# Optimization experiments

Hardware: AMD Instinct MI355X
Metric: run time of the kernel (lower is better)

Reference implementation:

```python
import jax, jax.numpy as jnp
import numpy as np

B, D, C, L, H, HF, HG, NCLS = 4096, 2048, 16, 128, 256, 512, 128, 200

def _init(key, shape, fan_in):
    return jax.random.normal(key, shape, dtype=jnp.float32) * (1.0 / np.sqrt(fan_in))

def setup_inputs() -> dict:
    key = jax.random.key(0)
    ks = jax.random.split(key, 16)
    return {
        "x": jax.random.normal(ks[0], (B, D), dtype=jnp.float32),
        "fp": jax.random.uniform(ks[1], (C, D), minval=-1.0, maxval=1.0, dtype=jnp.float32),  # probability_vector_logits
        "mean_inputs": jax.random.normal(ks[2], (D,), dtype=jnp.float32) * 0.1,
        "Wg1": _init(ks[3], (C, D, H), D), "bg1": jnp.zeros((C, H), jnp.float32),
        "Wg2": _init(ks[4], (C, H, L), H), "bg2": jnp.zeros((C, L), jnp.float32),
        "Wf1": _init(ks[5], (D, HF), D), "bf1": jnp.zeros((HF,), jnp.float32),
        "Wf2": _init(ks[6], (HF, L), HF), "bf2": jnp.zeros((L,), jnp.float32),
        "Wg_head": _init(ks[7], (C * (L // 2), HG), C * (L // 2)), "bg_head": jnp.zeros((HG,), jnp.float32),
        "Wc": _init(ks[8], (HG, NCLS), HG), "bc": jnp.zeros((NCLS,), jnp.float32),
    }

def _l2_normalize(v, axis):
    # tf.math.l2_normalize: v * rsqrt(max(sum(v^2), 1e-12))
    sq = jnp.sum(v * v, axis=axis, keepdims=True)
    return v * jax.lax.rsqrt(jnp.maximum(sq, 1e-12))

def reference(x, fp, mean_inputs, Wg1, bg1, Wg2, bg2, Wf1, bf1, Wf2, bf2, Wg_head, bg_head, Wc, bc):
    # Deterministic forward (training=False, forward_deterministic=True)
    gate = jax.nn.sigmoid(fp)  # [C, D]
    # mask_features: gate*x + (1-gate)*mean, vectorized over concepts -> [C, B, D]
    masked = gate[:, None, :] * x[None, :, :] + (1.0 - gate)[:, None, :] * mean_inputs[None, None, :]
    # per-concept generator MLPs (distinct weights per concept) -> concept_matrix [B, C, L]
    h = jax.nn.relu(jnp.einsum('cbd,cdh->cbh', masked, Wg1) + bg1[:, None, :])
    cm = jnp.einsum('cbh,chl->cbl', h, Wg2) + bg2[:, None, :]
    cm = jnp.transpose(cm, (1, 0, 2))              # [B, C, L]
    cm_norm = _l2_normalize(cm, axis=1)            # normalize across concept axis (axis=1 in TF code)
    # shared features_to_concepts model applied to each masked_x -> latent [C, B, L]
    hf = jax.nn.relu(jnp.einsum('cbd,dh->cbh', masked, Wf1) + bf1)
    latent = jnp.einsum('cbh,hl->cbl', hf, Wf2) + bf2
    latent = jnp.transpose(latent, (1, 0, 2))      # [B, C, L]
    # concept scores: sigmoid(<cm_norm[b,c,:], latent[b,c,:]>)
    concept_prob = jax.nn.sigmoid(jnp.sum(cm_norm * latent, axis=-1))  # [B, C]
    half = L // 2
    p = concept_prob[:, :, None]
    bottleneck = p * cm_norm[:, :, half:] + (1.0 - p) * cm_norm[:, :, :half]  # [B, C, L/2]
    bottleneck = bottleneck.reshape(bottleneck.shape[0], -1)                   # [B, C*L/2]
    # g_model + concepts_to_labels head
    z = jax.nn.relu(bottleneck @ Wg_head + bg_head)
    logits = z @ Wc + bc  # [B, NCLS]
    return logits
```

## Files before the change

kernel.cpp:

```cpp
#include <hip/hip_runtime.h>
#include <hip/hip_bf16.h>

typedef __bf16 bf16;
typedef __attribute__((ext_vector_type(8))) __bf16 bf16x8;
typedef __attribute__((ext_vector_type(4))) float f32x4;

__device__ __forceinline__ void gload_lds16(const void* g, void* l) {
    __builtin_amdgcn_global_load_lds(
        (const __attribute__((address_space(1))) unsigned int*)g,
        (__attribute__((address_space(3))) unsigned int*)l, 16, 0, 0);
}

#define BARRIER()   asm volatile("s_barrier" ::: "memory")
#define WAITLGKM0() asm volatile("s_waitcnt lgkmcnt(0)" ::: "memory")
#define WAITVM4()   asm volatile("s_waitcnt vmcnt(4)" ::: "memory")
#define WAITVM0()   asm volatile("s_waitcnt vmcnt(0)" ::: "memory")
#define SCHED0()    __builtin_amdgcn_sched_barrier(0)

__device__ __forceinline__ unsigned int pack2(float a, float b) {
    bf16 x = (bf16)a, y = (bf16)b;
    unsigned short ux, uy;
    __builtin_memcpy(&ux, &x, 2); __builtin_memcpy(&uy, &y, 2);
    return (unsigned int)ux | ((unsigned int)uy << 16);
}


__global__ void cvt_x(const float* __restrict__ in, bf16* __restrict__ out) {
    const long i = ((long)blockIdx.x * 256 + threadIdx.x) * 8;
    float4 v0 = *(const float4*)(in + i);
    float4 v1 = *(const float4*)(in + i + 4);
    bf16x8 o;
    o[0]=(bf16)v0.x; o[1]=(bf16)v0.y; o[2]=(bf16)v0.z; o[3]=(bf16)v0.w;
    o[4]=(bf16)v1.x; o[5]=(bf16)v1.y; o[6]=(bf16)v1.z; o[7]=(bf16)v1.w;
    *(bf16x8*)(out + i) = o;
}

__global__ void prep_gmv(const float* __restrict__ fp, const float* __restrict__ mean,
                         float* __restrict__ gmv) {
    const int i = blockIdx.x * 256 + threadIdx.x;
    const float g = 1.f / (1.f + expf(-fp[i]));
    gmv[i] = (1.f - g) * mean[i & 2047];
}

template <int SHARED_W>
__global__ void corr_kernel(const float* __restrict__ W, const float* __restrict__ gmv,
                            float* __restrict__ corr, int S) {
    __shared__ float red[4][64];
    const int c = blockIdx.y;
    const int sl = threadIdx.x & 63;
    const int s = blockIdx.x * 64 + sl;
    const int w = threadIdx.x >> 6;
    const float* Wc = W + (SHARED_W ? 0 : (long)c * 2048 * S);
    const float* gm = gmv + c * 2048;
    float acc = 0.f;
#pragma unroll 4
    for (int r = w; r < 2048; r += 4)
        acc = fmaf(gm[r], Wc[(long)r * S + s], acc);
    red[w][sl] = acc;
    __syncthreads();
    if (w == 0)
        corr[(long)c * S + s] = red[0][sl] + red[1][sl] + red[2][sl] + red[3][sl];
}

__global__ void prep_big(const float* __restrict__ Wg1, const float* __restrict__ Wf1,
                         bf16* __restrict__ Wall, const float* __restrict__ fp)
{
    __shared__ float tile[32][33];
    const int z = blockIdx.z;
    const int bx = blockIdx.x;
    const int r0 = blockIdx.y * 32;
    const int tx = threadIdx.x & 31, ty = threadIdx.x >> 5;
    const float* in; bf16* out; int S, s0;
    if (bx < 8) { S = 256; s0 = bx * 32; in = Wg1 + (long)z * 2048 * 256;
                  out = Wall + (long)z * 768 * 2048; }
    else        { S = 512; s0 = (bx - 8) * 32; in = Wf1;
                  out = Wall + (long)z * 768 * 2048 + (long)256 * 2048; }
#pragma unroll
    for (int i = 0; i < 32; i += 8)
        tile[ty + i][tx] = in[(long)(r0 + ty + i) * S + s0 + tx];
    __syncthreads();
    const float gv = 1.f / (1.f + expf(-fp[z * 2048 + r0 + tx]));
#pragma unroll
    for (int i = 0; i < 32; i += 8)
        out[(long)(s0 + ty + i) * 2048 + r0 + tx] = (bf16)(gv * tile[tx][ty + i]);
}

__global__ void prep_small(const float* __restrict__ Wg2, bf16* __restrict__ Wg2T,
                           const float* __restrict__ Wf2, bf16* __restrict__ Wf2T,
                           const float* __restrict__ Wgh, bf16* __restrict__ WghT)
{
    __shared__ float tile[32][33];
    const int b = blockIdx.x;
    const float* in; bf16* out; int R, bx, by;
    if (b < 512) {
        const int z = b >> 5, rem = b & 31;
        bx = rem & 3; by = rem >> 2; R = 256;
        in = Wg2 + (long)z * 256 * 128; out = Wg2T + (long)z * 128 * 256;
    } else if (b < 576) {
        const int rem = b - 512;
        bx = rem & 3; by = rem >> 2; R = 512;
        in = Wf2; out = Wf2T;
    } else {
        const int rem = b - 576;
        bx = rem & 3; by = rem >> 2; R = 1024;
        in = Wgh; out = WghT;
    }
    const int s0 = bx * 32, r0 = by * 32;
    const int tx = threadIdx.x & 31, ty = threadIdx.x >> 5;
#pragma unroll
    for (int i = 0; i < 32; i += 8)
        tile[ty + i][tx] = in[(long)(r0 + ty + i) * 128 + s0 + tx];
    __syncthreads();
#pragma unroll
    for (int i = 0; i < 32; i += 8)
        out[(long)(s0 + ty + i) * R + r0 + tx] = (bf16)tile[tx][ty + i];
}

__global__ __launch_bounds__(512, 2)
void gemm256(const bf16* __restrict__ A, const bf16* __restrict__ Wall,
             const float* __restrict__ bg1, const float* __restrict__ corr_g,
             const float* __restrict__ bf1, const float* __restrict__ corr_f,
             bf16* __restrict__ h_out, bf16* __restrict__ hf_out)
{
    __shared__ __align__(16) bf16 lds[2][4][8192];

    const int bid = blockIdx.x;
    const int swz = (bid & 7) * 96 + (bid >> 3);
    const int c   = swz / 48;
    const int rem = swz % 48;
    const int ny  = rem / 16;
    const int m0  = (rem % 16) * 256;

    const int t = threadIdx.x, lane = t & 63, w = t >> 6;
    const int wr = w >> 2, wc = w & 3;
    const bf16* Bc = Wall + (long)c * 768 * 2048;

    const int rr = lane >> 3;
    const int qq = (lane & 7) ^ rr;
    const bf16* pA0 = A  + (long)(m0 + w * 16 + rr) * 2048 + qq * 8;
    const bf16* pA1 = pA0 + 8 * 2048;
    const bf16* pB0 = Bc + (long)(ny * 256 + w * 16 + rr) * 2048 + qq * 8;
    const bf16* pB1 = pB0 + 8 * 2048;

    const int l15 = lane & 15;
    const int q0 = (((lane >> 4) ^ (lane & 7))) * 8;
    const int aoff0 = l15 * 64 + q0, aoff1 = aoff0 ^ 32;
    const int boff0 = ((wc & 1) * 64 + l15) * 64 + q0, boff1 = boff0 ^ 32;
    const int hb = 2 + (wc >> 1);

    f32x4 acc[8][4] = {};
    bf16x8 Ax[4][2], Ay[4][2], Bx[2][2], By[2][2];

#define STG(buf, half, P0, P1, e) do { \
    gload_lds16((P0) + (e), &lds[buf][half][w * 1024]); \
    gload_lds16((P1) + (e), &lds[buf][half][w * 1024 + 512]); } while (0)

#define RDA(dst, buf, mb) do { _Pragma("unroll") \
    for (int mm = 0; mm < 4; ++mm) { \
        dst[mm][0] = *(const bf16x8*)&lds[buf][wr][aoff0 + (mb + mm) * 1024]; \
        dst[mm][1] = *(const bf16x8*)&lds[buf][wr][aoff1 + (mb + mm) * 1024]; } } while (0)

#define RDB(dst, buf, nh) do { _Pragma("unroll") \
    for (int nn = 0; nn < 2; ++nn) { \
        dst[nn][0] = *(const bf16x8*)&lds[buf][hb][boff0 + (nh * 2 + nn) * 1024]; \
        dst[nn][1] = *(const bf16x8*)&lds[buf][hb][boff1 + (nh * 2 + nn) * 1024]; } } while (0)

#define MFMA16(mb, Af, Bf, nh) do { __builtin_amdgcn_s_setprio(1); _Pragma("unroll") \
    for (int kk = 0; kk < 2; ++kk) { _Pragma("unroll") \
      for (int mm = 0; mm < 4; ++mm) { _Pragma("unroll") \
        for (int nn = 0; nn < 2; ++nn) { \
            acc[mb + mm][nh * 2 + nn] = __builtin_amdgcn_mfma_f32_16x16x32_bf16( \
                Af[mm][kk], Bf[nn][kk], acc[mb + mm][nh * 2 + nn], 0, 0, 0); } } } \
    __builtin_amdgcn_s_setprio(0); } while (0)

    STG(0, 0, pA0, pA1, 0);
    STG(0, 1, pA0, pA1, 262144);
    STG(0, 2, pB0, pB1, 0);
    STG(0, 3, pB0, pB1, 262144);
    STG(1, 2, pB0, pB1, 64);
    STG(1, 3, pB0, pB1, 262144 + 64);
    WAITVM4();
    BARRIER();
    RDA(Ax, 0, 0); RDB(Bx, 0, 0);

#pragma unroll 1
    for (int it = 0; it < 15; ++it) {
        const int kB  = (2 * it + 1) * 64;
        const int kA2 = (2 * it + 2) * 64;
        const int kB2 = (2 * it + 3) * 64;
        STG(1, 0, pA0, pA1, kB);
        BARRIER();
        RDB(By, 0, 1);
        SCHED0();
        MFMA16(0, Ax, Bx, 0);
        BARRIER();
        STG(1, 1, pA0, pA1, 262144 + kB);
        BARRIER();
        RDA(Ay, 0, 4);
        SCHED0();
        MFMA16(0, Ax, By, 1);
        BARRIER();
        STG(0, 2, pB0, pB1, kA2);
        BARRIER();
        MFMA16(4, Ay, By, 1);
        BARRIER();
        STG(0, 3, pB0, pB1, 262144 + kA2);
        WAITVM4();
        BARRIER();
        RDA(Ax, 1, 0);
        SCHED0();
        MFMA16(4, Ay, Bx, 0);
        RDB(Bx, 1, 0);
        BARRIER();
        STG(0, 0, pA0, pA1, kA2);
        BARRIER();
        RDB(By, 1, 1);
        SCHED0();
        MFMA16(0, Ax, Bx, 0);
        BARRIER();
        STG(0, 1, pA0, pA1, 262144 + kA2);
        BARRIER();
        RDA(Ay, 1, 4);
        SCHED0();
        MFMA16(0, Ax, By, 1);
        BARRIER();
        STG(1, 2, pB0, pB1, kB2);
        BARRIER();
        MFMA16(4, Ay, By, 1);
        BARRIER();
        STG(1, 3, pB0, pB1, 262144 + kB2);
        WAITVM4();
        BARRIER();
        RDA(Ax, 0, 0);
        SCHED0();
        MFMA16(4, Ay, Bx, 0);
        RDB(Bx, 0, 0);
        BARRIER();
    }

    {
        const int kB = 31 * 64;
        STG(1, 0, pA0, pA1, kB);
        BARRIER();
        RDB(By, 0, 1);
        SCHED0();
        MFMA16(0, Ax, Bx, 0);
        BARRIER();
        STG(1, 1, pA0, pA1, 262144 + kB);
        BARRIER();
        RDA(Ay, 0, 4);
        SCHED0();
        MFMA16(0, Ax, By, 1);
        BARRIER();
        MFMA16(4, Ay, By, 1);
        BARRIER();
        WAITVM0();
        BARRIER();
        RDA(Ax, 1, 0);
        SCHED0();
        MFMA16(4, Ay, Bx, 0);
        RDB(Bx, 1, 0);
        BARRIER();
        RDB(By, 1, 1);
        SCHED0();
        MFMA16(0, Ax, Bx, 0);
        BARRIER();
        RDA(Ay, 1, 4);
        SCHED0();
        MFMA16(0, Ax, By, 1);
        BARRIER();
        MFMA16(4, Ay, By, 1);
        MFMA16(4, Ay, Bx, 0);
    }

    WAITLGKM0();
    BARRIER();
    bf16* cst = (bf16*)&lds[0][0][0];
    const int r4 = (lane >> 4) * 4;
    const int isH = (ny == 0);
    const int N = isH ? 256 : 512;
#pragma unroll
    for (int n = 0; n < 4; ++n) {
        const int cl = wc * 64 + n * 16 + l15;
        float bv;
        if (isH) bv = bg1[c * 256 + cl] + corr_g[c * 256 + cl];
        else {
            const int cf = (ny - 1) * 256 + cl;
            bv = bf1[cf] + corr_f[c * 512 + cf];
        }
#pragma unroll
        for (int m = 0; m < 8; ++m)
#pragma unroll
            for (int j = 0; j < 4; ++j) {
                const int row = wr * 128 + m * 16 + r4 + j;
                cst[row * 256 + cl] = (bf16)fmaxf(acc[m][n][j] + bv, 0.0f);
            }
    }
    BARRIER();
    bf16* obase = isH ? h_out + ((long)c * 4096 + m0) * 256
                      : hf_out + ((long)c * 4096 + m0) * 512 + (ny - 1) * 256;
    const int trow = t >> 5, tch = (t & 31) * 8;
#pragma unroll
    for (int pass = 0; pass < 16; ++pass) {
        const int row = pass * 16 + trow;
        *(bf16x8*)&obase[(long)row * N + tch] = *(const bf16x8*)&cst[row * 256 + tch];
    }
#undef STG
#undef RDA
#undef RDB
#undef MFMA16
}

__global__ __launch_bounds__(256, 2)
void gemm_mid(const bf16* __restrict__ h, const bf16* __restrict__ hf,
              const bf16* __restrict__ Wg2T, const bf16* __restrict__ Wf2T,
              const float* __restrict__ bg2, const float* __restrict__ bf2,
              bf16* __restrict__ cm, bf16* __restrict__ lat)
{
    __shared__ __align__(16) bf16 As[128 * 64];
    __shared__ __align__(16) bf16 Bs[128 * 64];

    const int z  = blockIdx.z;
    const int m0 = blockIdx.x * 128;
    const int t  = threadIdx.x;
    const int lane = t & 63, wave = t >> 6;
    const int wr = wave >> 1, wc = wave & 1;

    int K; const bf16 *Ac, *W; const float* bias; bf16* outp;
    if (z < 16) {
        K = 256; Ac = h + (long)z * 4096 * 256; W = Wg2T + (long)z * 128 * 256;
        bias = bg2 + z * 128; outp = cm + (long)m0 * 2048 + z * 128;
    } else {
        const int c = z - 16;
        K = 512; Ac = hf + (long)c * 4096 * 512; W = Wf2T;
        bias = bf2; outp = lat + (long)m0 * 2048 + c * 128;
    }

    const int sr = t >> 3;
    const int sc = (t & 7) * 8;

    f32x4 acc[4][4] = {};

    for (int kt = 0; kt < K / 64; ++kt) {
        const int k0 = kt * 64;
#pragma unroll
        for (int i = 0; i < 4; ++i)
            gload_lds16(Ac + (long)(m0 + i * 32 + sr) * K + k0 + sc, &As[i * 2048 + wave * 512]);
#pragma unroll
        for (int i = 0; i < 4; ++i)
            gload_lds16(W + (long)(i * 32 + sr) * K + k0 + sc, &Bs[i * 2048 + wave * 512]);
        __syncthreads();

#pragma unroll
        for (int kk = 0; kk < 2; ++kk) {
            bf16x8 af[4], bfr[4];
#pragma unroll
            for (int m = 0; m < 4; ++m)
                af[m] = *(const bf16x8*)&As[(wr * 64 + m * 16 + (lane & 15)) * 64 + kk * 32 + (lane >> 4) * 8];
#pragma unroll
            for (int n = 0; n < 4; ++n)
                bfr[n] = *(const bf16x8*)&Bs[(wc * 64 + n * 16 + (lane & 15)) * 64 + kk * 32 + (lane >> 4) * 8];
#pragma unroll
            for (int m = 0; m < 4; ++m)
#pragma unroll
                for (int n = 0; n < 4; ++n)
                    acc[m][n] = __builtin_amdgcn_mfma_f32_16x16x32_bf16(af[m], bfr[n], acc[m][n], 0, 0, 0);
        }
        __syncthreads();
    }

    const int ci = lane & 15, r4 = (lane >> 4) * 4;
#pragma unroll
    for (int m = 0; m < 4; ++m)
#pragma unroll
        for (int n = 0; n < 4; ++n) {
            const int col = wc * 64 + n * 16 + ci;
            const float bv = bias[col];
#pragma unroll
            for (int j = 0; j < 4; ++j) {
                const int row = wr * 64 + m * 16 + r4 + j;
                outp[(long)row * 2048 + col] = (bf16)(acc[m][n][j] + bv);
            }
        }
}

__global__ __launch_bounds__(256, 2)
void gemm_zp(const bf16* __restrict__ A, const bf16* __restrict__ Wt,
             float* __restrict__ outf)
{
    __shared__ __align__(16) bf16 As[128 * 64];
    __shared__ __align__(16) bf16 Bs[128 * 64];

    const int z  = blockIdx.z;
    const int m0 = blockIdx.x * 128;
    const int t  = threadIdx.x;
    const int lane = t & 63, wave = t >> 6;
    const int wr = wave >> 1, wc = wave & 1;

    const bf16* Ac = A  + (long)z * 128;
    const bf16* W  = Wt + (long)z * 128;
    float* outp = outf + (long)z * 4096 * 128 + (long)m0 * 128;

    const int sr = t >> 3;
    const int sc = (t & 7) * 8;

    f32x4 acc[4][4] = {};

    for (int kt = 0; kt < 2; ++kt) {
        const int k0 = kt * 64;
#pragma unroll
        for (int i = 0; i < 4; ++i)
            gload_lds16(Ac + (long)(m0 + i * 32 + sr) * 1024 + k0 + sc, &As[i * 2048 + wave * 512]);
#pragma unroll
        for (int i = 0; i < 4; ++i)
            gload_lds16(W + (long)(i * 32 + sr) * 1024 + k0 + sc, &Bs[i * 2048 + wave * 512]);
        __syncthreads();

#pragma unroll
        for (int kk = 0; kk < 2; ++kk) {
            bf16x8 af[4], bfr[4];
#pragma unroll
            for (int m = 0; m < 4; ++m)
                af[m] = *(const bf16x8*)&As[(wr * 64 + m * 16 + (lane & 15)) * 64 + kk * 32 + (lane >> 4) * 8];
#pragma unroll
            for (int n = 0; n < 4; ++n)
                bfr[n] = *(const bf16x8*)&Bs[(wc * 64 + n * 16 + (lane & 15)) * 64 + kk * 32 + (lane >> 4) * 8];
#pragma unroll
            for (int m = 0; m < 4; ++m)
#pragma unroll
                for (int n = 0; n < 4; ++n)
                    acc[m][n] = __builtin_amdgcn_mfma_f32_16x16x32_bf16(af[m], bfr[n], acc[m][n], 0, 0, 0);
        }
        __syncthreads();
    }

    const int ci = lane & 15, r4 = (lane >> 4) * 4;
#pragma unroll
    for (int m = 0; m < 4; ++m)
#pragma unroll
        for (int n = 0; n < 4; ++n) {
            const int col = wc * 64 + n * 16 + ci;
#pragma unroll
            for (int j = 0; j < 4; ++j) {
                const int row = wr * 64 + m * 16 + r4 + j;
                outp[(long)row * 128 + col] = acc[m][n][j];
            }
        }
}

__global__ void fuse_kernel(const unsigned int* __restrict__ cm, const unsigned int* __restrict__ lat,
                            unsigned int* __restrict__ bott)
{
    const int wave = threadIdx.x >> 6;
    const int l    = threadIdx.x & 63;
    const int b    = blockIdx.x * 4 + wave;
    const unsigned int* cu = cm  + (size_t)b * 1024;
    const unsigned int* lu = lat + (size_t)b * 1024;

    float c0[16], c1[16], l0[16], l1[16];
    float sq0 = 0.f, sq1 = 0.f;
#pragma unroll
    for (int c = 0; c < 16; ++c) {
        const unsigned int vc = cu[c * 64 + l], vl = lu[c * 64 + l];
        c0[c] = __uint_as_float(vc << 16);
        c1[c] = __uint_as_float(vc & 0xffff0000u);
        l0[c] = __uint_as_float(vl << 16);
        l1[c] = __uint_as_float(vl & 0xffff0000u);
        sq0 += c0[c] * c0[c]; sq1 += c1[c] * c1[c];
    }
    const float rs0 = rsqrtf(fmaxf(sq0, 1e-12f));
    const float rs1 = rsqrtf(fmaxf(sq1, 1e-12f));
#pragma unroll
    for (int c = 0; c < 16; ++c) {
        const float cn0 = c0[c] * rs0, cn1 = c1[c] * rs1;
        float part = cn0 * l0[c] + cn1 * l1[c];
#pragma unroll
        for (int off = 32; off; off >>= 1) part += __shfl_xor(part, off);
        const float p = 1.0f / (1.0f + expf(-part));
        const float o0 = __shfl_xor(cn0, 32), o1 = __shfl_xor(cn1, 32);
        if (l < 32)
            bott[(size_t)b * 512 + c * 32 + l] =
                pack2(p * o0 + (1.f - p) * cn0, p * o1 + (1.f - p) * cn1);
    }
}

__global__ void head2_kernel(const float* __restrict__ zp, const float* __restrict__ bgh,
                             const float* __restrict__ Wc, const float* __restrict__ bc,
                             float* __restrict__ out)
{
    __shared__ float zs[8][128];
    const int b0 = blockIdx.x * 8;
    const int t = threadIdx.x;
#pragma unroll
    for (int i = 0; i < 4; ++i) {
        const int idx = t + i * 256;
        const int r = idx >> 7, k = idx & 127;
        float s = bgh[k];
#pragma unroll
        for (int ks = 0; ks < 8; ++ks) s += zp[(size_t)ks * 524288 + (size_t)(b0 + r) * 128 + k];
        zs[r][k] = fmaxf(s, 0.0f);
    }
    __syncthreads();
    if (t < 200) {
        float a[8];
#pragma unroll
        for (int r = 0; r < 8; ++r) a[r] = bc[t];
        for (int k = 0; k < 128; ++k) {
            const float wv = Wc[k * 200 + t];
#pragma unroll
            for (int r = 0; r < 8; ++r) a[r] = fmaf(zs[r][k], wv, a[r]);
        }
#pragma unroll
        for (int r = 0; r < 8; ++r) out[(size_t)(b0 + r) * 200 + t] = a[r];
    }
}


extern "C" void kernel_launch(void* const* d_in, const int* in_sizes, int n_in,
                              void* d_out, int out_size, void* d_ws, size_t ws_size,
                              hipStream_t stream)
{
    (void)in_sizes; (void)n_in; (void)out_size; (void)ws_size;

    const float* x    = (const float*)d_in[0];
    const float* fp   = (const float*)d_in[1];
    const float* mean = (const float*)d_in[2];
    const float* Wg1  = (const float*)d_in[3];
    const float* bg1  = (const float*)d_in[4];
    const float* Wg2  = (const float*)d_in[5];
    const float* bg2  = (const float*)d_in[6];
    const float* Wf1  = (const float*)d_in[7];
    const float* bf1  = (const float*)d_in[8];
    const float* Wf2  = (const float*)d_in[9];
    const float* bf2  = (const float*)d_in[10];
    const float* Wgh  = (const float*)d_in[11];
    const float* bgh  = (const float*)d_in[12];
    const float* Wc   = (const float*)d_in[13];
    const float* bc   = (const float*)d_in[14];
    float* outp = (float*)d_out;

    char* p = (char*)d_ws;
    size_t off = 0;
    auto alloc = [&](size_t bytes) { void* r = p + off; off += (bytes + 255) & ~(size_t)255; return r; };
    bf16*  xbf    = (bf16*) alloc((size_t)4096 * 2048 * 2);
    bf16*  Wall   = (bf16*) alloc((size_t)16 * 768 * 2048 * 2);
    bf16*  Wg2T   = (bf16*) alloc((size_t)16 * 128 * 256 * 2);
    bf16*  Wf2T   = (bf16*) alloc((size_t)128 * 512 * 2);
    bf16*  WghT   = (bf16*) alloc((size_t)128 * 1024 * 2);
    float* gmv    = (float*)alloc((size_t)16 * 2048 * 4);
    float* corr_g = (float*)alloc((size_t)16 * 256 * 4);
    float* corr_f = (float*)alloc((size_t)16 * 512 * 4);
    bf16*  h      = (bf16*) alloc((size_t)16 * 4096 * 256 * 2);
    bf16*  hf     = (bf16*) alloc((size_t)16 * 4096 * 512 * 2);
    bf16*  cm     = (bf16*) alloc((size_t)4096 * 2048 * 2);
    bf16*  lat    = (bf16*) alloc((size_t)4096 * 2048 * 2);
    bf16*  bott   = (bf16*) alloc((size_t)4096 * 1024 * 2);
    float* zp     = (float*)alloc((size_t)8 * 4096 * 128 * 4);

    cvt_x<<<4096, 256, 0, stream>>>(x, xbf);
    prep_gmv<<<128, 256, 0, stream>>>(fp, mean, gmv);
    prep_big<<<dim3(24, 64, 16), 256, 0, stream>>>(Wg1, Wf1, Wall, fp);
    prep_small<<<704, 256, 0, stream>>>(Wg2, Wg2T, Wf2, Wf2T, Wgh, WghT);
    corr_kernel<0><<<dim3(4, 16), 256, 0, stream>>>(Wg1, gmv, corr_g, 256);
    corr_kernel<1><<<dim3(8, 16), 256, 0, stream>>>(Wf1, gmv, corr_f, 512);

    gemm256<<<768, 512, 0, stream>>>(xbf, Wall, bg1, corr_g, bf1, corr_f, h, hf);

    gemm_mid<<<dim3(32, 1, 32), 256, 0, stream>>>(h, hf, Wg2T, Wf2T, bg2, bf2, cm, lat);

    fuse_kernel<<<1024, 256, 0, stream>>>((const unsigned int*)cm, (const unsigned int*)lat,
                                          (unsigned int*)bott);

    gemm_zp<<<dim3(32, 1, 8), 256, 0, stream>>>(bott, WghT, zp);

    head2_kernel<<<512, 256, 0, stream>>>(zp, bgh, Wc, bc, outp);
}
```

Before: 362.8 us.

## Split weight prep kernels, fuse gate into corr, swizzle LDS stores, bf16 partials

Several independent changes. The prep_gmv kernel is removed and the gate computation is fused into corr_kernel. prep_big is split so the shared Wf1 tile is loaded once and written out for 8 concepts. The gemm256 epilogue LDS staging gets an XOR swizzle to reduce bank conflicts. The gemm_zp split-K partials are stored as bf16 instead of fp32, halving that traffic at some cost in precision. corr_kernel now recomputes a sigmoid per element, which adds redundant exp work.

```diff
diff --git a/kernel.cpp b/kernel.cpp
--- a/kernel.cpp
+++ b/kernel.cpp
@@ -35,15 +35,9 @@
     *(bf16x8*)(out + i) = o;
 }
 
-__global__ void prep_gmv(const float* __restrict__ fp, const float* __restrict__ mean,
-                         float* __restrict__ gmv) {
-    const int i = blockIdx.x * 256 + threadIdx.x;
-    const float g = 1.f / (1.f + expf(-fp[i]));
-    gmv[i] = (1.f - g) * mean[i & 2047];
-}
-
 template <int SHARED_W>
-__global__ void corr_kernel(const float* __restrict__ W, const float* __restrict__ gmv,
+__global__ void corr_kernel(const float* __restrict__ W, const float* __restrict__ fp,
+                            const float* __restrict__ mean,
                             float* __restrict__ corr, int S) {
     __shared__ float red[4][64];
     const int c = blockIdx.y;
@@ -51,38 +45,57 @@
     const int s = blockIdx.x * 64 + sl;
     const int w = threadIdx.x >> 6;
     const float* Wc = W + (SHARED_W ? 0 : (long)c * 2048 * S);
-    const float* gm = gmv + c * 2048;
+    const float* fpc = fp + c * 2048;
     float acc = 0.f;
 #pragma unroll 4
-    for (int r = w; r < 2048; r += 4)
-        acc = fmaf(gm[r], Wc[(long)r * S + s], acc);
+    for (int r = w; r < 2048; r += 4) {
+        const float g = 1.f / (1.f + expf(-fpc[r]));
+        acc = fmaf((1.f - g) * mean[r], Wc[(long)r * S + s], acc);
+    }
     red[w][sl] = acc;
     __syncthreads();
     if (w == 0)
         corr[(long)c * S + s] = red[0][sl] + red[1][sl] + red[2][sl] + red[3][sl];
 }
 
-__global__ void prep_big(const float* __restrict__ Wg1, const float* __restrict__ Wf1,
-                         bf16* __restrict__ Wall, const float* __restrict__ fp)
+__global__ void prep_wg1(const float* __restrict__ Wg1, bf16* __restrict__ Wall,
+                         const float* __restrict__ fp)
 {
     __shared__ float tile[32][33];
     const int z = blockIdx.z;
-    const int bx = blockIdx.x;
-    const int r0 = blockIdx.y * 32;
+    const int s0 = blockIdx.x * 32, r0 = blockIdx.y * 32;
     const int tx = threadIdx.x & 31, ty = threadIdx.x >> 5;
-    const float* in; bf16* out; int S, s0;
-    if (bx < 8) { S = 256; s0 = bx * 32; in = Wg1 + (long)z * 2048 * 256;
-                  out = Wall + (long)z * 768 * 2048; }
-    else        { S = 512; s0 = (bx - 8) * 32; in = Wf1;
-                  out = Wall + (long)z * 768 * 2048 + (long)256 * 2048; }
+    const float* in = Wg1 + (long)z * 2048 * 256;
+    bf16* out = Wall + (long)z * 768 * 2048;
 #pragma unroll
     for (int i = 0; i < 32; i += 8)
-        tile[ty + i][tx] = in[(long)(r0 + ty + i) * S + s0 + tx];
+        tile[ty + i][tx] = in[(long)(r0 + ty + i) * 256 + s0 + tx];
     __syncthreads();
     const float gv = 1.f / (1.f + expf(-fp[z * 2048 + r0 + tx]));
 #pragma unroll
     for (int i = 0; i < 32; i += 8)
         out[(long)(s0 + ty + i) * 2048 + r0 + tx] = (bf16)(gv * tile[tx][ty + i]);
+}
+
+__global__ void prep_wf1(const float* __restrict__ Wf1, bf16* __restrict__ Wall,
+                         const float* __restrict__ fp)
+{
+    __shared__ float tile[32][33];
+    const int s0 = blockIdx.x * 32, r0 = blockIdx.y * 32;
+    const int tx = threadIdx.x & 31, ty = threadIdx.x >> 5;
+#pragma unroll
+    for (int i = 0; i < 32; i += 8)
+        tile[ty + i][tx] = Wf1[(long)(r0 + ty + i) * 512 + s0 + tx];
+    __syncthreads();
+#pragma unroll 1
+    for (int zz = 0; zz < 8; ++zz) {
+        const int z = blockIdx.z * 8 + zz;
+        bf16* out = Wall + (long)z * 768 * 2048 + (long)256 * 2048;
+        const float gv = 1.f / (1.f + expf(-fp[z * 2048 + r0 + tx]));
+#pragma unroll
+        for (int i = 0; i < 32; i += 8)
+            out[(long)(s0 + ty + i) * 2048 + r0 + tx] = (bf16)(gv * tile[tx][ty + i]);
+    }
 }
 
 __global__ void prep_small(const float* __restrict__ Wg2, bf16* __restrict__ Wg2T,
@@ -293,7 +306,7 @@
 #pragma unroll
             for (int j = 0; j < 4; ++j) {
                 const int row = wr * 128 + m * 16 + r4 + j;
-                cst[row * 256 + cl] = (bf16)fmaxf(acc[m][n][j] + bv, 0.0f);
+                cst[row * 256 + (cl ^ ((row & 3) << 4))] = (bf16)fmaxf(acc[m][n][j] + bv, 0.0f);
             }
     }
     BARRIER();
@@ -303,7 +316,8 @@
 #pragma unroll
     for (int pass = 0; pass < 16; ++pass) {
         const int row = pass * 16 + trow;
-        *(bf16x8*)&obase[(long)row * N + tch] = *(const bf16x8*)&cst[row * 256 + tch];
+        *(bf16x8*)&obase[(long)row * N + tch] =
+            *(const bf16x8*)&cst[row * 256 + (tch ^ ((row & 3) << 4))];
     }
 #undef STG
 #undef RDA
@@ -386,7 +400,7 @@
 
 __global__ __launch_bounds__(256, 2)
 void gemm_zp(const bf16* __restrict__ A, const bf16* __restrict__ Wt,
-             float* __restrict__ outf)
+             bf16* __restrict__ outb)
 {
     __shared__ __align__(16) bf16 As[128 * 64];
     __shared__ __align__(16) bf16 Bs[128 * 64];
@@ -399,7 +413,7 @@
 
     const bf16* Ac = A  + (long)z * 128;
     const bf16* W  = Wt + (long)z * 128;
-    float* outp = outf + (long)z * 4096 * 128 + (long)m0 * 128;
+    bf16* outp = outb + (long)z * 4096 * 128 + (long)m0 * 128;
 
     const int sr = t >> 3;
     const int sc = (t & 7) * 8;
@@ -443,7 +457,7 @@
 #pragma unroll
             for (int j = 0; j < 4; ++j) {
                 const int row = wr * 64 + m * 16 + r4 + j;
-                outp[(long)row * 128 + col] = acc[m][n][j];
+                outp[(long)row * 128 + col] = (bf16)acc[m][n][j];
             }
         }
 }
@@ -484,7 +498,7 @@
     }
 }
 
-__global__ void head2_kernel(const float* __restrict__ zp, const float* __restrict__ bgh,
+__global__ void head2_kernel(const bf16* __restrict__ zp, const float* __restrict__ bgh,
                              const float* __restrict__ Wc, const float* __restrict__ bc,
                              float* __restrict__ out)
 {
@@ -497,7 +511,8 @@
         const int r = idx >> 7, k = idx & 127;
         float s = bgh[k];
 #pragma unroll
-        for (int ks = 0; ks < 8; ++ks) s += zp[(size_t)ks * 524288 + (size_t)(b0 + r) * 128 + k];
+        for (int ks = 0; ks < 8; ++ks)
+            s += (float)zp[(size_t)ks * 524288 + (size_t)(b0 + r) * 128 + k];
         zs[r][k] = fmaxf(s, 0.0f);
     }
     __syncthreads();
@@ -547,7 +562,6 @@
     bf16*  Wg2T   = (bf16*) alloc((size_t)16 * 128 * 256 * 2);
     bf16*  Wf2T   = (bf16*) alloc((size_t)128 * 512 * 2);
     bf16*  WghT   = (bf16*) alloc((size_t)128 * 1024 * 2);
-    float* gmv    = (float*)alloc((size_t)16 * 2048 * 4);
     float* corr_g = (float*)alloc((size_t)16 * 256 * 4);
     float* corr_f = (float*)alloc((size_t)16 * 512 * 4);
     bf16*  h      = (bf16*) alloc((size_t)16 * 4096 * 256 * 2);
@@ -555,14 +569,14 @@
     bf16*  cm     = (bf16*) alloc((size_t)4096 * 2048 * 2);
     bf16*  lat    = (bf16*) alloc((size_t)4096 * 2048 * 2);
     bf16*  bott   = (bf16*) alloc((size_t)4096 * 1024 * 2);
-    float* zp     = (float*)alloc((size_t)8 * 4096 * 128 * 4);
+    bf16*  zp     = (bf16*) alloc((size_t)8 * 4096 * 128 * 2);
 
     cvt_x<<<4096, 256, 0, stream>>>(x, xbf);
-    prep_gmv<<<128, 256, 0, stream>>>(fp, mean, gmv);
-    prep_big<<<dim3(24, 64, 16), 256, 0, stream>>>(Wg1, Wf1, Wall, fp);
+    prep_wg1<<<dim3(8, 64, 16), 256, 0, stream>>>(Wg1, Wall, fp);
+    prep_wf1<<<dim3(16, 64, 2), 256, 0, stream>>>(Wf1, Wall, fp);
     prep_small<<<704, 256, 0, stream>>>(Wg2, Wg2T, Wf2, Wf2T, Wgh, WghT);
-    corr_kernel<0><<<dim3(4, 16), 256, 0, stream>>>(Wg1, gmv, corr_g, 256);
-    corr_kernel<1><<<dim3(8, 16), 256, 0, stream>>>(Wf1, gmv, corr_f, 512);
+    corr_kernel<0><<<dim3(4, 16), 256, 0, stream>>>(Wg1, fp, mean, corr_g, 256);
+    corr_kernel<1><<<dim3(8, 16), 256, 0, stream>>>(Wf1, fp, mean, corr_f, 512);
 
     gemm256<<<768, 512, 0, stream>>>(xbf, Wall, bg1, corr_g, bf1, corr_f, h, hf);
 
```

New measurement: 376.2 us. +3.7%, slower.
